# Optimization experiments

Hardware: AMD Instinct MI355X
Metric: run time of the kernel (lower is better)

## Reference

```python
import jax, jax.numpy as jnp
import numpy as np

TOP_K = 4  # config.num_experts_per_tok


def setup_inputs() -> dict:
    key = jax.random.key(0)
    ks = jax.random.split(key, 8)
    B, S, H = 1, 2048, 1024
    E, I = 16, 512          # n_routed_experts, moe_intermediate_size
    SI = 512 * 2            # shared expert intermediate = moe_inter * n_shared_experts
    w = 0.02                # weight init scale
    return {
        "hidden_states": jax.random.normal(ks[0], (B, S, H), jnp.float32),
        "gate_w": jax.random.normal(ks[1], (E, H), jnp.float32) * w,
        "expert_gate": jax.random.normal(ks[2], (E, H, I), jnp.float32) * w,
        "expert_up": jax.random.normal(ks[3], (E, H, I), jnp.float32) * w,
        "expert_down": jax.random.normal(ks[4], (E, I, H), jnp.float32) * w,
        "shared_gate": jax.random.normal(ks[5], (H, SI), jnp.float32) * w,
        "shared_up": jax.random.normal(ks[6], (H, SI), jnp.float32) * w,
        "shared_down": jax.random.normal(ks[7], (SI, H), jnp.float32) * w,
    }


def reference(hidden_states, gate_w, expert_gate, expert_up, expert_down,
              shared_gate, shared_up, shared_down):
    B, S, H = hidden_states.shape
    E = gate_w.shape[0]
    x = hidden_states.reshape(-1, H)                     # [T, H]
    T = x.shape[0]

    # ---- MoEGate: sigmoid scores, top-k, normalize weights ----
    scores = jax.nn.sigmoid(x @ gate_w.T)                # [T, E]
    topk_w, topk_idx = jax.lax.top_k(scores, TOP_K)      # [T, k]
    topk_w = topk_w / (topk_w.sum(-1, keepdims=True) + 1e-20)

    # dense combine matrix: combine[t, e] = sum_k topk_w[t,k] * (topk_idx[t,k]==e)
    combine = jnp.zeros((T, E), x.dtype).at[
        jnp.arange(T)[:, None], topk_idx].add(topk_w)    # [T, E]

    # ---- routed experts (SwiGLU), computed densely and masked by combine ----
    g = jax.nn.silu(jnp.einsum('th,ehi->tei', x, expert_gate))
    u = jnp.einsum('th,ehi->tei', x, expert_up)
    expert_out = jnp.einsum('tei,eih->teh', g * u, expert_down)  # [T, E, H]
    y = jnp.einsum('te,teh->th', combine, expert_out)    # weighted combine

    # ---- shared expert (SwiGLU on all tokens) ----
    sg = jax.nn.silu(x @ shared_gate)
    shared_out = (sg * (x @ shared_up)) @ shared_down    # [T, H]

    return (y + shared_out).reshape(B, S, H)
```

## Files before the change

kernel.cpp:

```cpp
#include <hip/hip_runtime.h>


#define T_TOK 2048
#define H_DIM 1024
#define E_NUM 16
#define I_DIM 512
#define SI_DIM 1024

typedef __bf16 bf16x8 __attribute__((ext_vector_type(8)));
typedef short short8 __attribute__((ext_vector_type(8)));
typedef float f32x4 __attribute__((ext_vector_type(4)));
typedef unsigned short u16;

struct alignas(8)  U16x4 { u16 x, y, z, w; };

__device__ __forceinline__ float bf2f(u16 u) {
    union { float f; unsigned int i; } v; v.i = ((unsigned int)u) << 16; return v.f;
}
__device__ __forceinline__ u16 f2bf(float f) {
    union { float f; unsigned int i; } v; v.f = f;
    unsigned int i = v.i;
    return (u16)((i + 0x7fffu + ((i >> 16) & 1u)) >> 16);
}

#define GLOAD16(g, l)                                                          \
    __builtin_amdgcn_global_load_lds(                                          \
        (const __attribute__((address_space(1))) unsigned int*)(const void*)(g),\
        (__attribute__((address_space(3))) unsigned int*)(void*)(l), 16, 0, 0)

#define CNT(e) ((e) * 16)

__device__ __forceinline__ void tr_tile(
    const float* __restrict__ in, u16* __restrict__ out,
    int R, int C, int z, int by, int bx)
{
    const long boff = (long)z * R * C;
    const int r0 = by * 64, c0 = bx * 64;
    const int q = threadIdx.x;
    const int r  = q & 63;
    const int cb = (q >> 6) * 16;

    const float* src = in  + boff + (long)(r0 + r) * C + (c0 + cb);
    u16*         dst = out + boff + (long)(c0 + cb) * R + (r0 + r);

#pragma unroll
    for (int p = 0; p < 4; ++p) {
        float4 v = *(const float4*)&src[p * 4];
        dst[(long)(p * 4 + 0) * R] = f2bf(v.x);
        dst[(long)(p * 4 + 1) * R] = f2bf(v.y);
        dst[(long)(p * 4 + 2) * R] = f2bf(v.z);
        dst[(long)(p * 4 + 3) * R] = f2bf(v.w);
    }
}

__device__ __forceinline__ void route_block(
    const float* __restrict__ x, const float* __restrict__ gw,
    int* __restrict__ cnt, int* __restrict__ tok,
    int* __restrict__ slot, float* __restrict__ wgt, u16* __restrict__ xb,
    int blk)
{
    const int wid  = threadIdx.x >> 6;
    const int lane = threadIdx.x & 63;
    const int t    = blk * 4 + wid;

    const float* xp = x + (long)t * H_DIM;
    float xr[16];
#pragma unroll
    for (int j = 0; j < 16; ++j) xr[j] = xp[lane + 64 * j];

#pragma unroll
    for (int j = 0; j < 16; ++j) xb[(long)t * H_DIM + lane + 64 * j] = f2bf(xr[j]);

    float sc[E_NUM];
#pragma unroll
    for (int e = 0; e < E_NUM; ++e) {
        const float* gp = gw + e * H_DIM;
        float d = 0.f;
#pragma unroll
        for (int j = 0; j < 16; ++j) d += xr[j] * gp[lane + 64 * j];
#pragma unroll
        for (int off = 32; off; off >>= 1) d += __shfl_xor(d, off);
        sc[e] = 1.f / (1.f + expf(-d));
    }

    float w[4]; int id[4];
    unsigned picked = 0;
    float sum = 0.f;
#pragma unroll
    for (int k = 0; k < 4; ++k) {
        float mv = -1.f; int mi = 0;
#pragma unroll
        for (int e = 0; e < E_NUM; ++e) {
            bool ok = !((picked >> e) & 1u) && (sc[e] > mv);
            mv = ok ? sc[e] : mv;
            mi = ok ? e : mi;
        }
        w[k] = mv; id[k] = mi; picked |= 1u << mi; sum += mv;
    }
    const float inv = 1.f / (sum + 1e-20f);

    if (lane == 0) {
#pragma unroll
        for (int k = 0; k < 4; ++k) {
            int pos = atomicAdd(&cnt[CNT(id[k])], 1);
            tok[id[k] * T_TOK + pos] = t;
            slot[t * 4 + k] = (id[k] << 16) | pos;
            wgt[t * 4 + k]  = w[k] * inv;
        }
    }
}

__global__ __launch_bounds__(256) void prep_kernel(
    const float* __restrict__ x,  const float* __restrict__ gw,
    const float* __restrict__ eg, const float* __restrict__ eu,
    const float* __restrict__ ed, const float* __restrict__ sg,
    const float* __restrict__ su, const float* __restrict__ sd,
    u16* __restrict__ egT, u16* __restrict__ euT, u16* __restrict__ edT,
    u16* __restrict__ sgT, u16* __restrict__ suT, u16* __restrict__ sdT,
    int* __restrict__ cnt, int* __restrict__ tok,
    int* __restrict__ slot, float* __restrict__ wgt, u16* __restrict__ xb)
{
    int b = blockIdx.x;
    if (b < 2048) {
        int z = b >> 7, rem = b & 127;
        tr_tile(eg, egT, H_DIM, I_DIM, z, rem >> 3, rem & 7);
    } else if (b < 4096) {
        int l = b - 2048; int z = l >> 7, rem = l & 127;
        tr_tile(eu, euT, H_DIM, I_DIM, z, rem >> 3, rem & 7);
    } else if (b < 6144) {
        int l = b - 4096; int z = l >> 7, rem = l & 127;
        tr_tile(ed, edT, I_DIM, H_DIM, z, rem >> 4, rem & 15);
    } else if (b < 6400) {
        int l = b - 6144;
        tr_tile(sg, sgT, H_DIM, SI_DIM, 0, l >> 4, l & 15);
    } else if (b < 6656) {
        int l = b - 6400;
        tr_tile(su, suT, H_DIM, SI_DIM, 0, l >> 4, l & 15);
    } else if (b < 6912) {
        int l = b - 6656;
        tr_tile(sd, sdT, SI_DIM, H_DIM, 0, l >> 4, l & 15);
    } else {
        route_block(x, gw, cnt, tok, slot, wgt, xb, b - 6912);
    }
}

__global__ __launch_bounds__(256, 3) void gemm_up(
    const u16* __restrict__ xb,
    const u16* __restrict__ Wr1, const u16* __restrict__ Wr2,
    const u16* __restrict__ Ws1, const u16* __restrict__ Ws2,
    u16* __restrict__ actR, u16* __restrict__ actS,
    const int* __restrict__ cnt, const int* __restrict__ tok)
{
    constexpr int NWG = 896, CPX = NWG / 8;
    const int bswz = blockIdx.x;
    int j = (bswz & 7) * CPX + (bswz >> 3);

    bool routed = false;
    int e = 0, mb = 0, nb = 0, M = 0, rbase = 0;
    {
        int acc = 0, found = 0;
        for (int i = 0; i < E_NUM && !found; ++i) {
            int m   = cnt[CNT(i)];
            int nbk = (m + 127) >> 7;
            int bl  = nbk * 8;
            if (j < bl) { routed = true; e = i; M = m; mb = j % nbk; nb = j / nbk; found = 1; }
            else        { j -= bl; acc += m; }
        }
        rbase = acc;
        if (!routed) {
            if (j >= 256) return;
            M = T_TOK; mb = j & 15; nb = j >> 4;
        }
    }

    const u16 *B1p, *B2p;
    int Ntot;
    if (routed) {
        Ntot = I_DIM;
        B1p  = Wr1 + (long)e * (512L * 1024L);
        B2p  = Wr2 + (long)e * (512L * 1024L);
    } else {
        Ntot = SI_DIM;
        B1p = Ws1; B2p = Ws2;
    }
    const int m0 = mb * 128;
    const int n0 = nb * 64;
    const int K  = H_DIM;

    __shared__ __attribute__((aligned(16))) u16 sA[128 * 64];
    __shared__ __attribute__((aligned(16))) u16 sB1[64 * 64];
    __shared__ __attribute__((aligned(16))) u16 sB2[64 * 64];

    const int tid  = threadIdx.x;
    const int lane = tid & 63;
    const int wid  = tid >> 6;
    const int wr   = wid >> 1;
    const int wc   = wid & 1;

    const u16* aptr[4];
#pragma unroll
    for (int i = 0; i < 4; ++i) {
        int q = i * 256 + tid;
        int row = q >> 3, s = q & 7;
        int r = m0 + row; if (r >= M) r = M - 1;
        long grow = routed ? (long)tok[e * T_TOK + r] : (long)r;
        aptr[i] = xb + grow * (long)K + ((s ^ (row & 7)) << 3);
    }
    const u16* bptr1[2]; const u16* bptr2[2];
#pragma unroll
    for (int i = 0; i < 2; ++i) {
        int q = i * 256 + tid;
        int row = q >> 3, s = q & 7;
        long go = (long)(n0 + row) * K + ((s ^ (row & 7)) << 3);
        bptr1[i] = B1p + go;
        bptr2[i] = B2p + go;
    }

    f32x4 accG[4][2], accU[4][2];
#pragma unroll
    for (int i = 0; i < 4; ++i)
#pragma unroll
        for (int jj = 0; jj < 2; ++jj) {
            accG[i][jj] = (f32x4){0.f, 0.f, 0.f, 0.f};
            accU[i][jj] = (f32x4){0.f, 0.f, 0.f, 0.f};
        }

    for (int kt = 0; kt < K; kt += 64) {
        __syncthreads();
#pragma unroll
        for (int i = 0; i < 4; ++i) GLOAD16(aptr[i] + kt, &sA[(i * 256 + tid) * 8]);
#pragma unroll
        for (int i = 0; i < 2; ++i) {
            GLOAD16(bptr1[i] + kt, &sB1[(i * 256 + tid) * 8]);
            GLOAD16(bptr2[i] + kt, &sB2[(i * 256 + tid) * 8]);
        }
        asm volatile("s_waitcnt vmcnt(0)" ::: "memory");
        __syncthreads();

#pragma unroll
        for (int ks = 0; ks < 2; ++ks) {
            bf16x8 a[4], bg[2], bu[2];
#pragma unroll
            for (int mf = 0; mf < 4; ++mf) {
                int row = wr * 64 + mf * 16 + (lane & 15);
                int c   = ks * 4 + (lane >> 4);
                a[mf] = __builtin_bit_cast(bf16x8,
                    *(const short8*)&sA[row * 64 + ((c ^ (row & 7)) << 3)]);
            }
#pragma unroll
            for (int nf = 0; nf < 2; ++nf) {
                int row = wc * 32 + nf * 16 + (lane & 15);
                int c   = ks * 4 + (lane >> 4);
                int o   = row * 64 + ((c ^ (row & 7)) << 3);
                bg[nf] = __builtin_bit_cast(bf16x8, *(const short8*)&sB1[o]);
                bu[nf] = __builtin_bit_cast(bf16x8, *(const short8*)&sB2[o]);
            }
#pragma unroll
            for (int mf = 0; mf < 4; ++mf)
#pragma unroll
                for (int nf = 0; nf < 2; ++nf) {
                    accG[mf][nf] = __builtin_amdgcn_mfma_f32_16x16x32_bf16(
                        a[mf], bg[nf], accG[mf][nf], 0, 0, 0);
                    accU[mf][nf] = __builtin_amdgcn_mfma_f32_16x16x32_bf16(
                        a[mf], bu[nf], accU[mf][nf], 0, 0, 0);
                }
        }
    }

    u16* outp = routed ? actR : actS;
#pragma unroll
    for (int mf = 0; mf < 4; ++mf)
#pragma unroll
        for (int nf = 0; nf < 2; ++nf)
#pragma unroll
            for (int r = 0; r < 4; ++r) {
                int row = m0 + wr * 64 + mf * 16 + (lane >> 4) * 4 + r;
                if (row >= M) continue;
                int col = n0 + wc * 32 + nf * 16 + (lane & 15);
                float g = accG[mf][nf][r];
                float v = g / (1.f + expf(-g)) * accU[mf][nf][r];
                long orow = routed ? (long)(rbase + row) : (long)row;
                outp[orow * Ntot + col] = f2bf(v);
            }
}

__global__ __launch_bounds__(256, 3) void gemm_down(
    const u16* __restrict__ actR, const u16* __restrict__ actS,
    const u16* __restrict__ Wr,   const u16* __restrict__ Ws,
    u16* __restrict__ pair, float* __restrict__ out,
    const int* __restrict__ cnt)
{
    constexpr int NWG = 760, CPX = NWG / 8;
    const int bswz = blockIdx.x;
    int j = (bswz & 7) * CPX + (bswz >> 3);

    bool routed = false;
    int e = 0, mb = 0, nb = 0, M = 0, rbase = 0;
    {
        int acc = 0, found = 0;
        for (int i = 0; i < E_NUM && !found; ++i) {
            int m   = cnt[CNT(i)];
            int nbk = (m + 127) >> 7;
            int bl  = nbk * 8;
            if (j < bl) { routed = true; e = i; M = m; mb = j % nbk; nb = j / nbk; found = 1; }
            else        { j -= bl; acc += m; }
        }
        rbase = acc;
        if (!routed) {
            if (j >= 128) return;
            M = T_TOK; mb = j & 15; nb = j >> 4;
        }
    }

    int K;
    const u16 *Ap, *Bp;
    if (routed) {
        K  = I_DIM;
        Ap = actR;
        Bp = Wr + (long)e * (512L * 1024L);
    } else {
        K = SI_DIM;
        Ap = actS; Bp = Ws;
    }
    const int m0 = mb * 128;
    const int n0 = nb * 128;

    __shared__ __attribute__((aligned(16))) u16 sA[128 * 64];
    __shared__ __attribute__((aligned(16))) u16 sB[128 * 64];

    const int tid  = threadIdx.x;
    const int lane = tid & 63;
    const int wid  = tid >> 6;
    const int wr   = wid >> 1;
    const int wc   = wid & 1;

    const u16* aptr[4];
#pragma unroll
    for (int i = 0; i < 4; ++i) {
        int q = i * 256 + tid;
        int row = q >> 3, s = q & 7;
        int r = m0 + row; if (r >= M) r = M - 1;
        long grow = routed ? (long)(rbase + r) : (long)r;
        aptr[i] = Ap + grow * (long)K + ((s ^ (row & 7)) << 3);
    }
    const u16* bptr[4];
#pragma unroll
    for (int i = 0; i < 4; ++i) {
        int q = i * 256 + tid;
        int row = q >> 3, s = q & 7;
        bptr[i] = Bp + (long)(n0 + row) * K + ((s ^ (row & 7)) << 3);
    }

    f32x4 acc[4][4];
#pragma unroll
    for (int i = 0; i < 4; ++i)
#pragma unroll
        for (int jj = 0; jj < 4; ++jj) acc[i][jj] = (f32x4){0.f, 0.f, 0.f, 0.f};

    for (int kt = 0; kt < K; kt += 64) {
        __syncthreads();
#pragma unroll
        for (int i = 0; i < 4; ++i) GLOAD16(aptr[i] + kt, &sA[(i * 256 + tid) * 8]);
#pragma unroll
        for (int i = 0; i < 4; ++i) GLOAD16(bptr[i] + kt, &sB[(i * 256 + tid) * 8]);
        asm volatile("s_waitcnt vmcnt(0)" ::: "memory");
        __syncthreads();

#pragma unroll
        for (int ks = 0; ks < 2; ++ks) {
            bf16x8 a[4], b[4];
#pragma unroll
            for (int mf = 0; mf < 4; ++mf) {
                int row = wr * 64 + mf * 16 + (lane & 15);
                int c   = ks * 4 + (lane >> 4);
                a[mf] = __builtin_bit_cast(bf16x8,
                    *(const short8*)&sA[row * 64 + ((c ^ (row & 7)) << 3)]);
            }
#pragma unroll
            for (int nf = 0; nf < 4; ++nf) {
                int row = wc * 64 + nf * 16 + (lane & 15);
                int c   = ks * 4 + (lane >> 4);
                b[nf] = __builtin_bit_cast(bf16x8,
                    *(const short8*)&sB[row * 64 + ((c ^ (row & 7)) << 3)]);
            }
#pragma unroll
            for (int mf = 0; mf < 4; ++mf)
#pragma unroll
                for (int nf = 0; nf < 4; ++nf)
                    acc[mf][nf] = __builtin_amdgcn_mfma_f32_16x16x32_bf16(
                        a[mf], b[nf], acc[mf][nf], 0, 0, 0);
        }
    }

#pragma unroll
    for (int mf = 0; mf < 4; ++mf)
#pragma unroll
        for (int nf = 0; nf < 4; ++nf)
#pragma unroll
            for (int r = 0; r < 4; ++r) {
                int row = m0 + wr * 64 + mf * 16 + (lane >> 4) * 4 + r;
                if (row >= M) continue;
                int col = n0 + wc * 64 + nf * 16 + (lane & 15);
                float v = acc[mf][nf][r];
                if (routed) pair[(long)(rbase + row) * H_DIM + col] = f2bf(v);
                else        out[(long)row * H_DIM + col] = v;
            }
}

__global__ __launch_bounds__(256) void combine_kernel(
    float* __restrict__ out, const u16* __restrict__ pair,
    const int* __restrict__ slot, const float* __restrict__ wgt,
    const int* __restrict__ cnt)
{
    __shared__ int eb_s[E_NUM];
    if (threadIdx.x < E_NUM) {
        int s = 0;
        for (int i = 0; i < E_NUM; ++i) s += (i < (int)threadIdx.x) ? cnt[CNT(i)] : 0;
        eb_s[threadIdx.x] = s;
    }
    __syncthreads();

    const int t = blockIdx.x;
    const int c = threadIdx.x * 4;
    float4 o = *(float4*)&out[(long)t * H_DIM + c];
#pragma unroll
    for (int k = 0; k < 4; ++k) {
        int s = slot[t * 4 + k];
        int e = s >> 16, pos = s & 0xffff;
        float w = wgt[t * 4 + k];
        const u16* pr = pair + (long)(eb_s[e] + pos) * H_DIM + c;
        U16x4 pv = *(const U16x4*)pr;
        o.x += w * bf2f(pv.x);
        o.y += w * bf2f(pv.y);
        o.z += w * bf2f(pv.z);
        o.w += w * bf2f(pv.w);
    }
    *(float4*)&out[(long)t * H_DIM + c] = o;
}

extern "C" void kernel_launch(void* const* d_in, const int* in_sizes, int n_in,
                              void* d_out, int out_size, void* d_ws, size_t ws_size,
                              hipStream_t stream)
{
    const float* x  = (const float*)d_in[0];
    const float* gw = (const float*)d_in[1];
    const float* eg = (const float*)d_in[2];
    const float* eu = (const float*)d_in[3];
    const float* ed = (const float*)d_in[4];
    const float* sg = (const float*)d_in[5];
    const float* su = (const float*)d_in[6];
    const float* sd = (const float*)d_in[7];
    float* out = (float*)d_out;

    unsigned char* w = (unsigned char*)d_ws;
    size_t off = 0;
    auto alloc = [&](size_t b) -> void* {
        off = (off + 255) & ~(size_t)255;
        void* p = w + off; off += b; return p;
    };
    int*   cnt  = (int*)  alloc(256 * 4);
    int*   tok  = (int*)  alloc((size_t)E_NUM * T_TOK * 4);
    int*   slot = (int*)  alloc((size_t)T_TOK * 4 * 4);
    float* wgt  = (float*)alloc((size_t)T_TOK * 4 * 4);
    u16*   xb   = (u16*)  alloc((size_t)T_TOK * H_DIM * 2);
    u16*   egT  = (u16*)  alloc((size_t)E_NUM * I_DIM * H_DIM * 2);
    u16*   euT  = (u16*)  alloc((size_t)E_NUM * I_DIM * H_DIM * 2);
    u16*   edT  = (u16*)  alloc((size_t)E_NUM * H_DIM * I_DIM * 2);
    u16*   sgT  = (u16*)  alloc((size_t)SI_DIM * H_DIM * 2);
    u16*   suT  = (u16*)  alloc((size_t)SI_DIM * H_DIM * 2);
    u16*   sdT  = (u16*)  alloc((size_t)H_DIM * SI_DIM * 2);
    u16*   actR = (u16*)  alloc((size_t)T_TOK * 4 * I_DIM * 2);
    u16*   actS = (u16*)  alloc((size_t)T_TOK * SI_DIM * 2);
    u16*   pair = (u16*)  alloc((size_t)T_TOK * 4 * H_DIM * 2);

    hipMemsetAsync(cnt, 0, 256 * 4, stream);

    prep_kernel<<<7424, 256, 0, stream>>>(x, gw, eg, eu, ed, sg, su, sd,
                                          egT, euT, edT, sgT, suT, sdT,
                                          cnt, tok, slot, wgt, xb);
    gemm_up<<<896, 256, 0, stream>>>(xb, egT, euT, sgT, suT,
                                     actR, actS, cnt, tok);
    gemm_down<<<760, 256, 0, stream>>>(actR, actS, edT, sdT,
                                       pair, out, cnt);
    combine_kernel<<<T_TOK, 256, 0, stream>>>(out, pair, slot, wgt, cnt);
}
```

Baseline: 249.1 us.

## Drop weight transposes; convert in place and transpose while staging into LDS

```diff
diff --git a/kernel.cpp b/kernel.cpp
--- a/kernel.cpp
+++ b/kernel.cpp
@@ -9,6 +9,7 @@
 
 typedef __bf16 bf16x8 __attribute__((ext_vector_type(8)));
 typedef short short8 __attribute__((ext_vector_type(8)));
+typedef unsigned short ushort8 __attribute__((ext_vector_type(8)));
 typedef float f32x4 __attribute__((ext_vector_type(4)));
 typedef unsigned short u16;
 
@@ -29,29 +30,6 @@
         (__attribute__((address_space(3))) unsigned int*)(void*)(l), 16, 0, 0)
 
 #define CNT(e) ((e) * 16)
-
-__device__ __forceinline__ void tr_tile(
-    const float* __restrict__ in, u16* __restrict__ out,
-    int R, int C, int z, int by, int bx)
-{
-    const long boff = (long)z * R * C;
-    const int r0 = by * 64, c0 = bx * 64;
-    const int q = threadIdx.x;
-    const int r  = q & 63;
-    const int cb = (q >> 6) * 16;
-
-    const float* src = in  + boff + (long)(r0 + r) * C + (c0 + cb);
-    u16*         dst = out + boff + (long)(c0 + cb) * R + (r0 + r);
-
-#pragma unroll
-    for (int p = 0; p < 4; ++p) {
-        float4 v = *(const float4*)&src[p * 4];
-        dst[(long)(p * 4 + 0) * R] = f2bf(v.x);
-        dst[(long)(p * 4 + 1) * R] = f2bf(v.y);
-        dst[(long)(p * 4 + 2) * R] = f2bf(v.z);
-        dst[(long)(p * 4 + 3) * R] = f2bf(v.w);
-    }
-}
 
 __device__ __forceinline__ void route_block(
     const float* __restrict__ x, const float* __restrict__ gw,
@@ -110,37 +88,54 @@
     }
 }
 
+#define NCHUNK 7077888L
+
 __global__ __launch_bounds__(256) void prep_kernel(
     const float* __restrict__ x,  const float* __restrict__ gw,
     const float* __restrict__ eg, const float* __restrict__ eu,
     const float* __restrict__ ed, const float* __restrict__ sg,
     const float* __restrict__ su, const float* __restrict__ sd,
-    u16* __restrict__ egT, u16* __restrict__ euT, u16* __restrict__ edT,
-    u16* __restrict__ sgT, u16* __restrict__ suT, u16* __restrict__ sdT,
+    u16* __restrict__ egb, u16* __restrict__ eub, u16* __restrict__ edb,
+    u16* __restrict__ sgb, u16* __restrict__ sub, u16* __restrict__ sdb,
     int* __restrict__ cnt, int* __restrict__ tok,
     int* __restrict__ slot, float* __restrict__ wgt, u16* __restrict__ xb)
 {
-    int b = blockIdx.x;
+    const int b = blockIdx.x;
     if (b < 2048) {
-        int z = b >> 7, rem = b & 127;
-        tr_tile(eg, egT, H_DIM, I_DIM, z, rem >> 3, rem & 7);
-    } else if (b < 4096) {
-        int l = b - 2048; int z = l >> 7, rem = l & 127;
-        tr_tile(eu, euT, H_DIM, I_DIM, z, rem >> 3, rem & 7);
-    } else if (b < 6144) {
-        int l = b - 4096; int z = l >> 7, rem = l & 127;
-        tr_tile(ed, edT, I_DIM, H_DIM, z, rem >> 4, rem & 15);
-    } else if (b < 6400) {
-        int l = b - 6144;
-        tr_tile(sg, sgT, H_DIM, SI_DIM, 0, l >> 4, l & 15);
-    } else if (b < 6656) {
-        int l = b - 6400;
-        tr_tile(su, suT, H_DIM, SI_DIM, 0, l >> 4, l & 15);
-    } else if (b < 6912) {
-        int l = b - 6656;
-        tr_tile(sd, sdT, SI_DIM, H_DIM, 0, l >> 4, l & 15);
+        for (long c = (long)b * 256 + threadIdx.x; c < NCHUNK; c += 2048L * 256) {
+            const float* src; u16* dst; long o;
+            if      (c < 2097152L) { src = eg; dst = egb; o = c; }
+            else if (c < 4194304L) { src = eu; dst = eub; o = c - 2097152L; }
+            else if (c < 6291456L) { src = ed; dst = edb; o = c - 4194304L; }
+            else if (c < 6553600L) { src = sg; dst = sgb; o = c - 6291456L; }
+            else if (c < 6815744L) { src = su; dst = sub; o = c - 6553600L; }
+            else                   { src = sd; dst = sdb; o = c - 6815744L; }
+            float4 v = *(const float4*)&src[o * 4];
+            U16x4 w = { f2bf(v.x), f2bf(v.y), f2bf(v.z), f2bf(v.w) };
+            *(U16x4*)&dst[o * 4] = w;
+        }
     } else {
-        route_block(x, gw, cnt, tok, slot, wgt, xb, b - 6912);
+        route_block(x, gw, cnt, tok, slot, wgt, xb, b - 2048);
+    }
+}
+
+__device__ __forceinline__ void stage_bt(
+    u16* __restrict__ lds, const u16* __restrict__ Wbase,
+    long ldn, int tid, int nbase)
+{
+    const int p    = tid & 31;
+    const int bk   = p * 2;
+    const int bn   = nbase + (tid >> 5) * 8;
+    const ushort8 v0 = *(const ushort8*)(Wbase + (long)bk * ldn);
+    const ushort8 v1 = *(const ushort8*)(Wbase + (long)(bk + 1) * ldn);
+    const int cp   = bk >> 3;
+    const int klo  = bk & 7;
+#pragma unroll
+    for (int j = 0; j < 8; ++j) {
+        int n   = bn + j;
+        int off = n * 64 + ((cp ^ (n & 7)) << 3) + klo;
+        *(unsigned int*)&lds[off] =
+            (unsigned int)v0[j] | ((unsigned int)v1[j] << 16);
     }
 }
 
@@ -174,13 +169,14 @@
     }
 
     const u16 *B1p, *B2p;
-    int Ntot;
+    long ldn;
+    int  Ntot;
     if (routed) {
-        Ntot = I_DIM;
+        Ntot = I_DIM; ldn = I_DIM;
         B1p  = Wr1 + (long)e * (512L * 1024L);
         B2p  = Wr2 + (long)e * (512L * 1024L);
     } else {
-        Ntot = SI_DIM;
+        Ntot = SI_DIM; ldn = SI_DIM;
         B1p = Ws1; B2p = Ws2;
     }
     const int m0 = mb * 128;
@@ -206,15 +202,8 @@
         long grow = routed ? (long)tok[e * T_TOK + r] : (long)r;
         aptr[i] = xb + grow * (long)K + ((s ^ (row & 7)) << 3);
     }
-    const u16* bptr1[2]; const u16* bptr2[2];
-#pragma unroll
-    for (int i = 0; i < 2; ++i) {
-        int q = i * 256 + tid;
-        int row = q >> 3, s = q & 7;
-        long go = (long)(n0 + row) * K + ((s ^ (row & 7)) << 3);
-        bptr1[i] = B1p + go;
-        bptr2[i] = B2p + go;
-    }
+    const u16* b1row = B1p + n0 + (tid >> 5) * 8;
+    const u16* b2row = B2p + n0 + (tid >> 5) * 8;
 
     f32x4 accG[4][2], accU[4][2];
 #pragma unroll
@@ -229,11 +218,8 @@
         __syncthreads();
 #pragma unroll
         for (int i = 0; i < 4; ++i) GLOAD16(aptr[i] + kt, &sA[(i * 256 + tid) * 8]);
-#pragma unroll
-        for (int i = 0; i < 2; ++i) {
-            GLOAD16(bptr1[i] + kt, &sB1[(i * 256 + tid) * 8]);
-            GLOAD16(bptr2[i] + kt, &sB2[(i * 256 + tid) * 8]);
-        }
+        stage_bt(sB1, b1row + (long)kt * ldn, ldn, tid, 0);
+        stage_bt(sB2, b2row + (long)kt * ldn, ldn, tid, 0);
         asm volatile("s_waitcnt vmcnt(0)" ::: "memory");
         __syncthreads();
 
@@ -322,6 +308,7 @@
         K = SI_DIM;
         Ap = actS; Bp = Ws;
     }
+    const long ldn = H_DIM;
     const int m0 = mb * 128;
     const int n0 = nb * 128;
 
@@ -343,13 +330,7 @@
         long grow = routed ? (long)(rbase + r) : (long)r;
         aptr[i] = Ap + grow * (long)K + ((s ^ (row & 7)) << 3);
     }
-    const u16* bptr[4];
-#pragma unroll
-    for (int i = 0; i < 4; ++i) {
-        int q = i * 256 + tid;
-        int row = q >> 3, s = q & 7;
-        bptr[i] = Bp + (long)(n0 + row) * K + ((s ^ (row & 7)) << 3);
-    }
+    const u16* brow = Bp + n0 + (tid >> 5) * 8;
 
     f32x4 acc[4][4];
 #pragma unroll
@@ -361,8 +342,8 @@
         __syncthreads();
 #pragma unroll
         for (int i = 0; i < 4; ++i) GLOAD16(aptr[i] + kt, &sA[(i * 256 + tid) * 8]);
-#pragma unroll
-        for (int i = 0; i < 4; ++i) GLOAD16(bptr[i] + kt, &sB[(i * 256 + tid) * 8]);
+        stage_bt(sB, brow + (long)kt * ldn, ldn, tid, 0);
+        stage_bt(sB, brow + (long)kt * ldn + 64, ldn, tid, 64);
         asm volatile("s_waitcnt vmcnt(0)" ::: "memory");
         __syncthreads();
 
@@ -463,24 +444,24 @@
     int*   slot = (int*)  alloc((size_t)T_TOK * 4 * 4);
     float* wgt  = (float*)alloc((size_t)T_TOK * 4 * 4);
     u16*   xb   = (u16*)  alloc((size_t)T_TOK * H_DIM * 2);
-    u16*   egT  = (u16*)  alloc((size_t)E_NUM * I_DIM * H_DIM * 2);
-    u16*   euT  = (u16*)  alloc((size_t)E_NUM * I_DIM * H_DIM * 2);
-    u16*   edT  = (u16*)  alloc((size_t)E_NUM * H_DIM * I_DIM * 2);
-    u16*   sgT  = (u16*)  alloc((size_t)SI_DIM * H_DIM * 2);
-    u16*   suT  = (u16*)  alloc((size_t)SI_DIM * H_DIM * 2);
-    u16*   sdT  = (u16*)  alloc((size_t)H_DIM * SI_DIM * 2);
+    u16*   egb  = (u16*)  alloc((size_t)E_NUM * H_DIM * I_DIM * 2);
+    u16*   eub  = (u16*)  alloc((size_t)E_NUM * H_DIM * I_DIM * 2);
+    u16*   edb  = (u16*)  alloc((size_t)E_NUM * I_DIM * H_DIM * 2);
+    u16*   sgb  = (u16*)  alloc((size_t)H_DIM * SI_DIM * 2);
+    u16*   sub  = (u16*)  alloc((size_t)H_DIM * SI_DIM * 2);
+    u16*   sdb  = (u16*)  alloc((size_t)SI_DIM * H_DIM * 2);
     u16*   actR = (u16*)  alloc((size_t)T_TOK * 4 * I_DIM * 2);
     u16*   actS = (u16*)  alloc((size_t)T_TOK * SI_DIM * 2);
     u16*   pair = (u16*)  alloc((size_t)T_TOK * 4 * H_DIM * 2);
 
     hipMemsetAsync(cnt, 0, 256 * 4, stream);
 
-    prep_kernel<<<7424, 256, 0, stream>>>(x, gw, eg, eu, ed, sg, su, sd,
-                                          egT, euT, edT, sgT, suT, sdT,
+    prep_kernel<<<2560, 256, 0, stream>>>(x, gw, eg, eu, ed, sg, su, sd,
+                                          egb, eub, edb, sgb, sub, sdb,
                                           cnt, tok, slot, wgt, xb);
-    gemm_up<<<896, 256, 0, stream>>>(xb, egT, euT, sgT, suT,
+    gemm_up<<<896, 256, 0, stream>>>(xb, egb, eub, sgb, sub,
                                      actR, actS, cnt, tok);
-    gemm_down<<<760, 256, 0, stream>>>(actR, actS, edT, sdT,
+    gemm_down<<<760, 256, 0, stream>>>(actR, actS, edb, sdb,
                                        pair, out, cnt);
     combine_kernel<<<T_TOK, 256, 0, stream>>>(out, pair, slot, wgt, cnt);
 }
```

Measured after the change: 297.7 us. 1.2x slower.
